# Kernel optimization log

Hardware: AMD Instinct MI355X
Metric: run time of the kernel (lower is better)

The kernel has to match this reference:

```python
import jax, jax.numpy as jnp
import numpy as np


def setup_inputs() -> dict:
    key = jax.random.key(0)
    k1, k2 = jax.random.split(key)
    N, D = 65536, 512
    feeds = jax.random.normal(k1, (N, D), dtype=jnp.float32)
    feeds_repeat_times = jax.random.randint(k2, (N,), 0, 8)
    return {
        "feeds": feeds,
        "feeds_repeat_times": feeds_repeat_times,
        "output_feeds_size": 262144,
    }


def reference(feeds, feeds_repeat_times, output_feeds_size):
    # Equivalent of the per-row repeat + cat + pad + truncate, as one fused gather.
    # Output row j comes from source row i where cumsum(repeats) first exceeds j.
    cum = jnp.cumsum(feeds_repeat_times)          # [N]
    total = cum[-1]                               # total repeated rows
    pos = jnp.arange(output_feeds_size)           # [S]
    idx = jnp.searchsorted(cum, pos, side="right")  # source row per output row
    valid = pos < total                           # rows beyond total are zero pad
    idx = jnp.clip(idx, 0, feeds.shape[0] - 1)
    out = jnp.where(valid[:, None], feeds[idx], jnp.zeros((), dtype=feeds.dtype))
    return out
```

## Files before the change

### kernel.cpp

```cpp
#include <hip/hip_runtime.h>

#define NROWS 65536
#define DCOLS 512
#define D4    128

typedef float f32x4 __attribute__((ext_vector_type(4)));

__global__ __launch_bounds__(1024) void scan_kernel(const int* __restrict__ rep,
                                                    int* __restrict__ cum) {
    __shared__ int sdata[1024];
    const int t = threadIdx.x;
    const int base = t * 64;

    int4 v[16];
    const int4* rep4 = (const int4*)(rep + base);
#pragma unroll
    for (int k = 0; k < 16; ++k) v[k] = rep4[k];

    int partial = 0;
#pragma unroll
    for (int k = 0; k < 16; ++k) partial += v[k].x + v[k].y + v[k].z + v[k].w;

    sdata[t] = partial;
    __syncthreads();
    for (int off = 1; off < 1024; off <<= 1) {
        int add = (t >= off) ? sdata[t - off] : 0;
        __syncthreads();
        sdata[t] += add;
        __syncthreads();
    }
    int running = sdata[t] - partial;

    int4* cum4 = (int4*)(cum + base);
#pragma unroll
    for (int k = 0; k < 16; ++k) {
        int4 x;
        running += v[k].x; x.x = running;
        running += v[k].y; x.y = running;
        running += v[k].z; x.z = running;
        running += v[k].w; x.w = running;
        cum4[k] = x;
    }
}

__global__ __launch_bounds__(256) void build_idx_kernel(const int* __restrict__ rep,
                                                        const int* __restrict__ cum,
                                                        int* __restrict__ idx,
                                                        int S) {
    const int i = blockIdx.x * blockDim.x + threadIdx.x;
    if (i >= NROWS) return;
    const int end   = cum[i];
    const int r     = rep[i];
    const int start = end - r;
    if (r == 0 || start >= S) return;
    const int stop = end < S ? end : S;
    for (int j = start; j < stop; ++j) idx[j] = i;
}

__global__ __launch_bounds__(256) void gather_kernel(const f32x4* __restrict__ feeds,
                                                     const int* __restrict__ idx,
                                                     const int* __restrict__ cum,
                                                     f32x4* __restrict__ out,
                                                     int S) {
    const int wave = (int)((blockIdx.x * blockDim.x + threadIdx.x) >> 6);
    const int lane = threadIdx.x & 63;
    if (wave >= S) return;

    const int total = cum[NROWS - 1];

    f32x4 a = (f32x4)0.f;
    f32x4 b = (f32x4)0.f;
    if (wave < total) {
        const int si = idx[wave];
        const f32x4* src = feeds + (long long)si * D4;
        a = src[lane];
        b = src[lane + 64];
    }
    f32x4* dst = out + (long long)wave * D4;
    __builtin_nontemporal_store(a, dst + lane);
    __builtin_nontemporal_store(b, dst + lane + 64);
}

extern "C" void kernel_launch(void* const* d_in, const int* in_sizes, int n_in,
                              void* d_out, int out_size, void* d_ws, size_t ws_size,
                              hipStream_t stream) {
    const float* feeds = (const float*)d_in[0];
    const int*   rep   = (const int*)d_in[1];
    const int S = out_size / DCOLS;

    int* cum = (int*)d_ws;
    int* idx = (int*)d_ws + NROWS;

    scan_kernel<<<1, 1024, 0, stream>>>(rep, cum);
    build_idx_kernel<<<NROWS / 256, 256, 0, stream>>>(rep, cum, idx, S);
    gather_kernel<<<S / 4, 256, 0, stream>>>((const f32x4*)feeds, idx, cum,
                                             (f32x4*)d_out, S);
}
```

Baseline: 609.0 us.

## Fuse index build and gather into per-source-row scatter expand kernel

Replaces the index-building kernel and the per-output-row gather with one kernel where each wave reads a source row once and writes it to all of its repeated output positions, then zero-fills the padded tail. This drops the intermediate index array, one kernel launch, and the repeated reads of the same source row. In exchange, per-wave work varies with the repeat count, which can cause load imbalance.

```diff
diff --git a/kernel.cpp b/kernel.cpp
--- a/kernel.cpp
+++ b/kernel.cpp
@@ -43,42 +43,38 @@
     }
 }
 
-__global__ __launch_bounds__(256) void build_idx_kernel(const int* __restrict__ rep,
-                                                        const int* __restrict__ cum,
-                                                        int* __restrict__ idx,
-                                                        int S) {
-    const int i = blockIdx.x * blockDim.x + threadIdx.x;
-    if (i >= NROWS) return;
-    const int end   = cum[i];
-    const int r     = rep[i];
-    const int start = end - r;
-    if (r == 0 || start >= S) return;
-    const int stop = end < S ? end : S;
-    for (int j = start; j < stop; ++j) idx[j] = i;
-}
-
-__global__ __launch_bounds__(256) void gather_kernel(const f32x4* __restrict__ feeds,
-                                                     const int* __restrict__ idx,
+__global__ __launch_bounds__(256) void expand_kernel(const f32x4* __restrict__ feeds,
+                                                     const int* __restrict__ rep,
                                                      const int* __restrict__ cum,
                                                      f32x4* __restrict__ out,
                                                      int S) {
     const int wave = (int)((blockIdx.x * blockDim.x + threadIdx.x) >> 6);
     const int lane = threadIdx.x & 63;
-    if (wave >= S) return;
+
+    const int i     = wave;
+    const int end   = cum[i];
+    const int r     = rep[i];
+    const int start = end - r;
+    const int stop  = end < S ? end : S;
+
+    if (start < stop) {
+        const f32x4* src = feeds + (long long)i * D4;
+        const f32x4 a = src[lane];
+        const f32x4 b = src[lane + 64];
+        for (int j = start; j < stop; ++j) {
+            f32x4* dst = out + (long long)j * D4;
+            __builtin_nontemporal_store(a, dst + lane);
+            __builtin_nontemporal_store(b, dst + lane + 64);
+        }
+    }
 
     const int total = cum[NROWS - 1];
-
-    f32x4 a = (f32x4)0.f;
-    f32x4 b = (f32x4)0.f;
-    if (wave < total) {
-        const int si = idx[wave];
-        const f32x4* src = feeds + (long long)si * D4;
-        a = src[lane];
-        b = src[lane + 64];
+    const f32x4 z = (f32x4)0.f;
+    for (int j = total + wave; j < S; j += NROWS) {
+        f32x4* dst = out + (long long)j * D4;
+        __builtin_nontemporal_store(z, dst + lane);
+        __builtin_nontemporal_store(z, dst + lane + 64);
     }
-    f32x4* dst = out + (long long)wave * D4;
-    __builtin_nontemporal_store(a, dst + lane);
-    __builtin_nontemporal_store(b, dst + lane + 64);
 }
 
 extern "C" void kernel_launch(void* const* d_in, const int* in_sizes, int n_in,
@@ -89,10 +85,8 @@
     const int S = out_size / DCOLS;
 
     int* cum = (int*)d_ws;
-    int* idx = (int*)d_ws + NROWS;
 
     scan_kernel<<<1, 1024, 0, stream>>>(rep, cum);
-    build_idx_kernel<<<NROWS / 256, 256, 0, stream>>>(rep, cum, idx, S);
-    gather_kernel<<<S / 4, 256, 0, stream>>>((const f32x4*)feeds, idx, cum,
-                                             (f32x4*)d_out, S);
+    expand_kernel<<<NROWS / 4, 256, 0, stream>>>((const f32x4*)feeds, rep, cum,
+                                                 (f32x4*)d_out, S);
 }
```

After: 640.2 us. 5.1% more time.
